# Kernel optimization log

Measured on AMD Instinct MI355X. Metric: run time of the kernel, lower is better.

Reference implementation:

```python
import jax, jax.numpy as jnp
import numpy as np

N, E, F, H, T, K = 50000, 800000, 128, 128, 10, 3


def setup_inputs() -> dict:
    key = jax.random.key(0)
    ks = jax.random.split(key, 12)
    def p(k, shape):
        return jax.random.normal(k, shape, dtype=jnp.float32) * 0.05
    inp = {
        "x": jax.random.normal(ks[0], (N, F), dtype=jnp.float32),
        "edge_index": jax.random.randint(ks[1], (2, E), 0, N, dtype=jnp.int64),
        "edge_weight": jax.random.uniform(ks[2], (E,), dtype=jnp.float32),
    }
    names = ["xz", "hz", "xr", "hr", "xh", "hh"]
    for i, nm in enumerate(names):
        cin = F if nm[0] == "x" else H
        inp["W" + nm] = p(ks[3 + i], (K, cin, H))  # ChebConv: K linear maps [in,out]
        inp["b" + nm] = jnp.zeros((H,), jnp.float32)
    inp["Wlin"] = p(ks[9], (H, T))
    inp["blin"] = jnp.zeros((T,), jnp.float32)
    return inp


def _cheb_norm(src, dst, edge_weight, n):
    # PyG ChebConv norm with normalization='sym', lambda_max=2.0:
    # L_hat = 2L/lambda_max - I = -D^{-1/2} A D^{-1/2}  (zero diagonal)
    deg = jax.ops.segment_sum(edge_weight, src, num_segments=n)
    deg_safe = jnp.where(deg > 0, deg, 1.0)
    dinv = jnp.where(deg > 0, jax.lax.rsqrt(deg_safe), 0.0)
    return -dinv[src] * edge_weight * dinv[dst]


def _cheb_conv(x, W, b, src, dst, norm, n):
    # out = sum_k T_k(L_hat) x @ W[k] + b, via Chebyshev recurrence
    def prop(t):  # L_hat @ t : gather from source nodes, scatter-add into targets
        return jax.ops.segment_sum(norm[:, None] * t[src], dst, num_segments=n)
    Tx0 = x
    out = Tx0 @ W[0]
    Tx1 = prop(Tx0)
    out = out + Tx1 @ W[1]
    for k in range(2, W.shape[0]):
        Tx2 = 2.0 * prop(Tx1) - Tx0
        out = out + Tx2 @ W[k]
        Tx0, Tx1 = Tx1, Tx2
    return out + b


def reference(x, edge_index, edge_weight, Wxz, bxz, Whz, bhz, Wxr, bxr,
              Whr, bhr, Wxh, bxh, Whh, bhh, Wlin, blin):
    n = x.shape[0]
    src, dst = edge_index[0], edge_index[1]
    norm = _cheb_norm(src, dst, edge_weight, n)
    Hs = jnp.zeros((n, Whz.shape[2]), x.dtype)  # GConvGRU inits H=None -> zeros
    Z = jax.nn.sigmoid(_cheb_conv(x, Wxz, bxz, src, dst, norm, n)
                       + _cheb_conv(Hs, Whz, bhz, src, dst, norm, n))
    R = jax.nn.sigmoid(_cheb_conv(x, Wxr, bxr, src, dst, norm, n)
                       + _cheb_conv(Hs, Whr, bhr, src, dst, norm, n))
    Ht = jnp.tanh(_cheb_conv(x, Wxh, bxh, src, dst, norm, n)
                  + _cheb_conv(Hs * R, Whh, bhh, src, dst, norm, n))
    Hn = Z * Hs + (1.0 - Z) * Ht
    return Hn @ Wlin + blin
```

## Files before the change

kernel.cpp:

```cpp
#include <hip/hip_runtime.h>
#include <hip/hip_fp16.h>

typedef __attribute__((ext_vector_type(8))) short bf16x8;
typedef __attribute__((ext_vector_type(4))) float f32x4;
typedef unsigned int u32;
typedef unsigned short u16;

#define CAP 48

static __device__ __forceinline__ u16 f2bf(float f) {
  u32 u = __float_as_uint(f);
  u32 r = (u + 0x7fffu + ((u >> 16) & 1u)) >> 16;
  return (u16)r;
}
static __device__ __forceinline__ u32 f2h15(float f) {
  __half h = __float2half(f);
  return (u32)(((__half_raw)h).x) & 0x7FFFu;
}
static __device__ __forceinline__ float h152f(u32 b) {
  __half_raw hr; hr.x = (u16)b;
  return __half2float(__half(hr));
}
static __device__ __forceinline__ void gload16(const void* g, void* l) {
  __builtin_amdgcn_global_load_lds((const __attribute__((address_space(1))) u32*)g,
                                   (__attribute__((address_space(3))) u32*)l, 16, 0, 0);
}

__global__ __launch_bounds__(256) void mega_kernel(
    const float* __restrict__ x, const int* __restrict__ ei, const float* __restrict__ w,
    const float* __restrict__ Wxz, const float* __restrict__ Wxh,
    const float* __restrict__ bxz, const float* __restrict__ bhz,
    const float* __restrict__ bxh, const float* __restrict__ bhh,
    u32* __restrict__ xw, float* __restrict__ deg, int* __restrict__ cur,
    u32* __restrict__ edges, u16* __restrict__ Bp, float* __restrict__ bzs,
    float* __restrict__ bhs, int E, int N, int nw, int eb, int pbBase, int interleave) {
  int bid = blockIdx.x, tid = threadIdx.x;
  if (bid >= pbBase) {
    int idx = (bid - pbBase) * 256 + tid;
    int j = idx & 7, h4 = (idx >> 3) & 3, n = (idx >> 5) & 15, ct = (idx >> 9) & 15, kt = idx >> 13;
    int k = kt * 32 + h4 * 8 + j;
    int c = ct * 16 + n;
    int kb = k >> 7, ci = k & 127, h = c >> 1;
    const float* W = (c & 1) ? Wxh : Wxz;
    float v = W[((size_t)kb * 128 + ci) * 128 + h];
    Bp[idx] = f2bf(v);
    if (idx < 128) { bzs[idx] = bxz[idx] + bhz[idx]; bhs[idx] = bxh[idx] + bhh[idx]; }
    return;
  }
  int role, g;
  if (interleave) { int r = bid % 6; g = bid / 6; role = (r >= 2) ? 2 : r; if (r >= 2) g = g * 4 + (r - 2); }
  else { if (bid < eb) { role = 0; g = bid; } else if (bid < 2 * eb) { role = 1; g = bid - eb; } else { role = 2; g = bid - 2 * eb; } }

  if (role == 2) {
    int i = g * 256 + tid;
    if (i < nw) {
      float2 v = *(const float2*)&x[(size_t)i * 2];
      xw[i] = (u32)f2bf(v.x) | ((u32)f2bf(v.y) << 16);
    }
  } else if (role == 0) {
    int e = g * 256 + tid;
    if (e < E) {
      int s = ei[e];
      if ((unsigned)s < (unsigned)N) atomicAdd(&deg[s], w[e]);
    }
  } else {
    int e = g * 256 + tid;
    if (e < E) {
      int s = ei[e], d = ei[E + e];
      if ((unsigned)s < (unsigned)N && (unsigned)d < (unsigned)N) {
        u32 rec = ((u32)s << 15) | f2h15(w[e]);
        int pos = atomicAdd(&cur[d], 1);
        if (pos < CAP) edges[d * CAP + pos] = rec;
      }
    }
  }
}

__global__ __launch_bounds__(256) void scale_kernel(const u32* __restrict__ xw,
                                                    const float* __restrict__ deg,
                                                    u32* __restrict__ xs, int N) {
  int node = (blockIdx.x << 2) + (threadIdx.x >> 6);
  if (node >= N) return;
  int lane = threadIdx.x & 63;
  float dd = deg[node];
  float di = dd > 0.f ? rsqrtf(dd) : 0.f;
  u32 v = xw[((unsigned)node << 6) | (unsigned)lane];
  float f0 = di * __uint_as_float(v << 16);
  float f1 = di * __uint_as_float(v & 0xffff0000u);
  xs[((unsigned)node << 6) | (unsigned)lane] = (u32)f2bf(f0) | ((u32)f2bf(f1) << 16);
}

#define ACC16(VV, NN)                                                   \
  _Pragma("unroll") for (int k_ = 0; k_ < 16; ++k_) {                   \
    a0 += NN[k_] * __uint_as_float(VV[k_] << 16);                       \
    a1 += NN[k_] * __uint_as_float(VV[k_] & 0xffff0000u);               \
  }

__global__ __launch_bounds__(256) void prop1_kernel(const u32* __restrict__ xs,
    const float* __restrict__ deg, const u32* __restrict__ edges, const int* __restrict__ cur,
    u32* __restrict__ t1w, u32* __restrict__ t1s, int N) {
  int node = (blockIdx.x << 2) + (threadIdx.x >> 6);
  if (node >= N) return;
  int lane = threadIdx.x & 63;
  int len = cur[node]; if (len > CAP) len = CAP;
  u32 my = edges[node * CAP + (lane < CAP ? lane : CAP - 1)];
  float a0 = 0.f, a1 = 0.f;
  u32 v[16]; float nv[16];
#pragma unroll
  for (int k = 0; k < 16; ++k) {
    u32 rec = (u32)__shfl((int)my, k);
    if (k < len) { v[k] = xs[((rec >> 15) << 6) | (unsigned)lane]; nv[k] = h152f(rec & 0x7FFFu); }
    else { v[k] = 0; nv[k] = 0.f; }
  }
  for (int base = 0; base < len; base += 16) {
    u32 vv[16]; float nn[16];
#pragma unroll
    for (int k = 0; k < 16; ++k) { vv[k] = v[k]; nn[k] = nv[k]; }
#pragma unroll
    for (int k = 0; k < 16; ++k) {
      int kn = base + 16 + k;
      u32 rec = (u32)__shfl((int)my, kn);
      if (kn < len) { v[k] = xs[((rec >> 15) << 6) | (unsigned)lane]; nv[k] = h152f(rec & 0x7FFFu); }
      else { v[k] = 0; nv[k] = 0.f; }
    }
    ACC16(vv, nn);
  }
  float dd = deg[node];
  float di = dd > 0.f ? rsqrtf(dd) : 0.f;
  float T0 = -di * a0, T1 = -di * a1;
  unsigned idx = ((unsigned)node << 6) | (unsigned)lane;
  t1w[idx] = (u32)f2bf(T0) | ((u32)f2bf(T1) << 16);
  t1s[idx] = (u32)f2bf(di * T0) | ((u32)f2bf(di * T1) << 16);
}

__global__ __launch_bounds__(256) void prop2_kernel(const u32* __restrict__ xw,
    const u32* __restrict__ t1s, const float* __restrict__ deg,
    const u32* __restrict__ edges, const int* __restrict__ cur,
    u32* __restrict__ t2w, int N) {
  int node = (blockIdx.x << 2) + (threadIdx.x >> 6);
  if (node >= N) return;
  int lane = threadIdx.x & 63;
  int len = cur[node]; if (len > CAP) len = CAP;
  u32 my = edges[node * CAP + (lane < CAP ? lane : CAP - 1)];
  float a0 = 0.f, a1 = 0.f;
  u32 v[16]; float nv[16];
#pragma unroll
  for (int k = 0; k < 16; ++k) {
    u32 rec = (u32)__shfl((int)my, k);
    if (k < len) { v[k] = t1s[((rec >> 15) << 6) | (unsigned)lane]; nv[k] = h152f(rec & 0x7FFFu); }
    else { v[k] = 0; nv[k] = 0.f; }
  }
  for (int base = 0; base < len; base += 16) {
    u32 vv[16]; float nn[16];
#pragma unroll
    for (int k = 0; k < 16; ++k) { vv[k] = v[k]; nn[k] = nv[k]; }
#pragma unroll
    for (int k = 0; k < 16; ++k) {
      int kn = base + 16 + k;
      u32 rec = (u32)__shfl((int)my, kn);
      if (kn < len) { v[k] = t1s[((rec >> 15) << 6) | (unsigned)lane]; nv[k] = h152f(rec & 0x7FFFu); }
      else { v[k] = 0; nv[k] = 0.f; }
    }
    ACC16(vv, nn);
  }
  float dd = deg[node];
  float di = dd > 0.f ? rsqrtf(dd) : 0.f;
  unsigned idx = ((unsigned)node << 6) | (unsigned)lane;
  u32 xv = xw[idx];
  float r0 = -2.f * di * a0 - __uint_as_float(xv << 16);
  float r1 = -2.f * di * a1 - __uint_as_float(xv & 0xffff0000u);
  t2w[idx] = (u32)f2bf(r0) | ((u32)f2bf(r1) << 16);
}

__global__ __launch_bounds__(512, 2) void gemm_kernel(
    const u16* __restrict__ xb, const u16* __restrict__ t1, const u16* __restrict__ t2,
    const u16* __restrict__ Bp, const float* __restrict__ bzs, const float* __restrict__ bhs,
    const float* __restrict__ Wlin, const float* __restrict__ blin,
    float* __restrict__ out, int N) {
  __shared__ __align__(16) char smem[49152];
  const int offB_[2] = {0, 16384};
  const int offA_[2] = {32768, 40960};

  int tid = threadIdx.x;
  int w = tid >> 6, lane = tid & 63;
  int l15 = lane & 15, lh = lane >> 4;
  int rowBase = blockIdx.x << 7;
  int wrow = (w >> 2) << 6;
  int wcol = (w & 3) << 6;

  const u16* acts[3] = {xb, t1, t2};

  f32x4 acc[4][4];
  f32x4 zero = {0.f, 0.f, 0.f, 0.f};
#pragma unroll
  for (int mi = 0; mi < 4; ++mi)
#pragma unroll
    for (int ni = 0; ni < 4; ++ni) acc[mi][ni] = zero;

  auto stageB = [&](int kt, int buf) {
    const char* g = (const char*)Bp + kt * 16384 + w * 2048 + lane * 16;
    char* l = smem + offB_[buf] + w * 2048;
    gload16(g, l);
    gload16(g + 1024, l + 1024);
  };
  auto stageA = [&](int kt, int buf) {
    int kb = kt >> 2;
    const u16* act = acts[kb];
    int rl = (w << 4) + (lane >> 2);
    int grow = rowBase + rl; if (grow >= N) grow = N - 1;
    int hsw = (lane & 3) ^ ((rl >> 1) & 3);
    const char* g = (const char*)act + (size_t)grow * 256 + ((kt & 3) << 6) + (hsw << 4);
    char* l = smem + offA_[buf] + (w << 10);
    gload16(g, l);
  };

  stageB(0, 0); stageA(0, 0);

#pragma unroll
  for (int kt = 0; kt < 12; ++kt) {
    __syncthreads();
    if (kt < 11) { stageB(kt + 1, (kt + 1) & 1); stageA(kt + 1, (kt + 1) & 1); }
    const char* Ab = smem + offA_[kt & 1];
    const char* Bb = smem + offB_[kt & 1];
    bf16x8 a[4], b[4];
#pragma unroll
    for (int mi = 0; mi < 4; ++mi) {
      int row = wrow + (mi << 4) + l15;
      int off = (row << 6) + ((lh ^ ((row >> 1) & 3)) << 4);
      a[mi] = *(const bf16x8*)(Ab + off);
    }
#pragma unroll
    for (int ni = 0; ni < 4; ++ni) {
      int ct = ((w & 3) << 2) + ni;
      int off = (((ct << 4) + l15) << 6) + (lh << 4);
      b[ni] = *(const bf16x8*)(Bb + off);
    }
#pragma unroll
    for (int mi = 0; mi < 4; ++mi)
#pragma unroll
      for (int ni = 0; ni < 4; ++ni)
        acc[mi][ni] = __builtin_amdgcn_mfma_f32_16x16x32_bf16(a[mi], b[ni], acc[mi][ni], 0, 0, 0);
  }

  __syncthreads();

  u16* HnS = (u16*)smem;
  float* WlS = (float*)(smem + 34816);
  float* blS = (float*)(smem + 34816 + 5120);
  for (int i = tid; i < 1280; i += 512) WlS[i] = Wlin[i];
  if (tid < 10) blS[tid] = blin[tid];

  int odd = lane & 1;
#pragma unroll
  for (int ni = 0; ni < 4; ++ni) {
    int h = (wcol + (ni << 4) + l15) >> 1;
    float badd = odd ? bhs[h] : bzs[h];
#pragma unroll
    for (int mi = 0; mi < 4; ++mi)
#pragma unroll
      for (int reg = 0; reg < 4; ++reg) {
        float pre = acc[mi][ni][reg] + badd;
        float s2 = odd ? 2.f * pre : pre;
        float e = __expf(s2);
        float A = odd ? 1.f : 0.f;
        float B = odd ? 2.f : -1.f;
        float r = A - B / (1.f + e);
        float o = __shfl_xor(r, 1);
        if (!odd) {
          int row = wrow + (mi << 4) + (lh << 2) + reg;
          HnS[row * 136 + h] = f2bf(r * o);
        }
      }
  }
  __syncthreads();

  for (int idx = tid; idx < 1280; idx += 512) {
    int row = idx / 10, t = idx - row * 10;
    int grow = rowBase + row;
    if (grow < N) {
      float s = blS[t];
      const u16* hr = HnS + row * 136;
#pragma unroll 4
      for (int hc = 0; hc < 16; ++hc) {
        uint4 q = *(const uint4*)(hr + (hc << 3));
        const float* wp = WlS + (hc << 3) * 10 + t;
        s += __uint_as_float(q.x << 16) * wp[0];
        s += __uint_as_float(q.x & 0xffff0000u) * wp[10];
        s += __uint_as_float(q.y << 16) * wp[20];
        s += __uint_as_float(q.y & 0xffff0000u) * wp[30];
        s += __uint_as_float(q.z << 16) * wp[40];
        s += __uint_as_float(q.z & 0xffff0000u) * wp[50];
        s += __uint_as_float(q.w << 16) * wp[60];
        s += __uint_as_float(q.w & 0xffff0000u) * wp[70];
      }
      out[(size_t)grow * 10 + t] = s;
    }
  }
}

extern "C" void kernel_launch(void* const* d_in, const int* in_sizes, int n_in,
                              void* d_out, int out_size, void* d_ws, size_t ws_size,
                              hipStream_t stream) {
  const float* x    = (const float*)d_in[0];
  const int*   ei   = (const int*)d_in[1];
  const float* w    = (const float*)d_in[2];
  const float* Wxz  = (const float*)d_in[3];
  const float* bxz  = (const float*)d_in[4];
  const float* bhz  = (const float*)d_in[6];
  const float* Wxh  = (const float*)d_in[11];
  const float* bxh  = (const float*)d_in[12];
  const float* bhh  = (const float*)d_in[14];
  const float* Wlin = (const float*)d_in[15];
  const float* blin = (const float*)d_in[16];
  float* out = (float*)d_out;

  int N = in_sizes[0] / 128;
  int E = in_sizes[2];

  char* p = (char*)d_ws;
  auto alloc = [&](size_t bytes) {
    char* r = p;
    p += (bytes + 255) & ~(size_t)255;
    return r;
  };
  float* deg   = (float*)alloc((size_t)N * 4);
  int*   cur   = (int*)alloc((size_t)N * 4);
  u32*   edges = (u32*)alloc((size_t)N * CAP * 4);
  u32*   xbw   = (u32*)alloc((size_t)N * 256);
  u32*   xs    = (u32*)alloc((size_t)N * 256);
  u32*   t1w   = (u32*)alloc((size_t)N * 256);
  u32*   t1s   = (u32*)alloc((size_t)N * 256);
  u32*   t2w   = (u32*)alloc((size_t)N * 256);
  u16*   Bp    = (u16*)alloc(196608);
  float* bzs   = (float*)alloc(512);
  float* bhs   = (float*)alloc(512);

  hipMemsetAsync(deg, 0, (size_t)N * 4, stream);
  hipMemsetAsync(cur, 0, (size_t)N * 4, stream);

  int nw = N * 64;
  int eb = (E + 255) / 256;
  int cb = (nw + 255) / 256;
  int interleave = (cb == 4 * eb) ? 1 : 0;
  int workB = interleave ? 6 * eb : (2 * eb + cb);
  int pbBase = workB;
  int grid = workB + 384;

  hipLaunchKernelGGL(mega_kernel, dim3(grid), dim3(256), 0, stream,
                     x, ei, w, Wxz, Wxh, bxz, bhz, bxh, bhh,
                     xbw, deg, cur, edges, Bp, bzs, bhs, E, N, nw, eb, pbBase, interleave);
  int nb = (N + 3) / 4;
  hipLaunchKernelGGL(scale_kernel, dim3(nb), dim3(256), 0, stream, xbw, deg, xs, N);
  hipLaunchKernelGGL(prop1_kernel, dim3(nb), dim3(256), 0, stream, xs, deg, edges, cur, t1w, t1s, N);
  hipLaunchKernelGGL(prop2_kernel, dim3(nb), dim3(256), 0, stream, xbw, t1s, deg, edges, cur, t2w, N);
  int gb = (N + 127) / 128;
  hipLaunchKernelGGL(gemm_kernel, dim3(gb), dim3(512), 0, stream,
                     (const u16*)xbw, (const u16*)t1w, (const u16*)t2w, Bp, bzs, bhs,
                     Wlin, blin, out, N);
}
```

Baseline: 295.5 us.

## Fold source-degree scaling into per-edge weights, drop scale kernel and t1s buffer

Each edge weight now absorbs the source node's inverse sqrt degree, computed once per lane before the gather loop. The propagation kernels can then read the unscaled bf16 features directly. This removes the separate scale pass, the pre-scaled xs copy, and the second t1s output write, which cuts one launch and several full N×128 bf16 read/write passes. It also merges the two memsets into one. In exchange, each edge does a random deg lookup and an rsqrt, and the rounding order changes slightly.

```diff
diff --git a/kernel.cpp b/kernel.cpp
--- a/kernel.cpp
+++ b/kernel.cpp
@@ -76,40 +76,30 @@
   }
 }
 
-__global__ __launch_bounds__(256) void scale_kernel(const u32* __restrict__ xw,
-                                                    const float* __restrict__ deg,
-                                                    u32* __restrict__ xs, int N) {
-  int node = (blockIdx.x << 2) + (threadIdx.x >> 6);
-  if (node >= N) return;
-  int lane = threadIdx.x & 63;
-  float dd = deg[node];
-  float di = dd > 0.f ? rsqrtf(dd) : 0.f;
-  u32 v = xw[((unsigned)node << 6) | (unsigned)lane];
-  float f0 = di * __uint_as_float(v << 16);
-  float f1 = di * __uint_as_float(v & 0xffff0000u);
-  xs[((unsigned)node << 6) | (unsigned)lane] = (u32)f2bf(f0) | ((u32)f2bf(f1) << 16);
-}
-
 #define ACC16(VV, NN)                                                   \
   _Pragma("unroll") for (int k_ = 0; k_ < 16; ++k_) {                   \
     a0 += NN[k_] * __uint_as_float(VV[k_] << 16);                       \
     a1 += NN[k_] * __uint_as_float(VV[k_] & 0xffff0000u);               \
   }
 
-__global__ __launch_bounds__(256) void prop1_kernel(const u32* __restrict__ xs,
+__global__ __launch_bounds__(256) void prop1_kernel(const u32* __restrict__ xw,
     const float* __restrict__ deg, const u32* __restrict__ edges, const int* __restrict__ cur,
-    u32* __restrict__ t1w, u32* __restrict__ t1s, int N) {
+    u32* __restrict__ t1w, int N) {
   int node = (blockIdx.x << 2) + (threadIdx.x >> 6);
   if (node >= N) return;
   int lane = threadIdx.x & 63;
   int len = cur[node]; if (len > CAP) len = CAP;
-  u32 my = edges[node * CAP + (lane < CAP ? lane : CAP - 1)];
+  u32 rec = edges[node * CAP + (lane < CAP ? lane : CAP - 1)];
+  u32 sbase = (rec >> 15) << 6;
+  float dgs = (lane < len) ? deg[rec >> 15] : 1.f;
+  float nvl = (lane < len && dgs > 0.f) ? h152f(rec & 0x7FFFu) * rsqrtf(dgs) : 0.f;
   float a0 = 0.f, a1 = 0.f;
   u32 v[16]; float nv[16];
 #pragma unroll
   for (int k = 0; k < 16; ++k) {
-    u32 rec = (u32)__shfl((int)my, k);
-    if (k < len) { v[k] = xs[((rec >> 15) << 6) | (unsigned)lane]; nv[k] = h152f(rec & 0x7FFFu); }
+    u32 sb = (u32)__shfl((int)sbase, k);
+    float n = __shfl(nvl, k);
+    if (k < len) { v[k] = xw[sb | (unsigned)lane]; nv[k] = n; }
     else { v[k] = 0; nv[k] = 0.f; }
   }
   for (int base = 0; base < len; base += 16) {
@@ -119,35 +109,38 @@
 #pragma unroll
     for (int k = 0; k < 16; ++k) {
       int kn = base + 16 + k;
-      u32 rec = (u32)__shfl((int)my, kn);
-      if (kn < len) { v[k] = xs[((rec >> 15) << 6) | (unsigned)lane]; nv[k] = h152f(rec & 0x7FFFu); }
+      u32 sb = (u32)__shfl((int)sbase, kn);
+      float n = __shfl(nvl, kn);
+      if (kn < len) { v[k] = xw[sb | (unsigned)lane]; nv[k] = n; }
       else { v[k] = 0; nv[k] = 0.f; }
     }
     ACC16(vv, nn);
   }
   float dd = deg[node];
-  float di = dd > 0.f ? rsqrtf(dd) : 0.f;
-  float T0 = -di * a0, T1 = -di * a1;
+  float di = dd > 0.f ? -rsqrtf(dd) : 0.f;
   unsigned idx = ((unsigned)node << 6) | (unsigned)lane;
-  t1w[idx] = (u32)f2bf(T0) | ((u32)f2bf(T1) << 16);
-  t1s[idx] = (u32)f2bf(di * T0) | ((u32)f2bf(di * T1) << 16);
+  t1w[idx] = (u32)f2bf(di * a0) | ((u32)f2bf(di * a1) << 16);
 }
 
 __global__ __launch_bounds__(256) void prop2_kernel(const u32* __restrict__ xw,
-    const u32* __restrict__ t1s, const float* __restrict__ deg,
+    const u32* __restrict__ t1w, const float* __restrict__ deg,
     const u32* __restrict__ edges, const int* __restrict__ cur,
     u32* __restrict__ t2w, int N) {
   int node = (blockIdx.x << 2) + (threadIdx.x >> 6);
   if (node >= N) return;
   int lane = threadIdx.x & 63;
   int len = cur[node]; if (len > CAP) len = CAP;
-  u32 my = edges[node * CAP + (lane < CAP ? lane : CAP - 1)];
+  u32 rec = edges[node * CAP + (lane < CAP ? lane : CAP - 1)];
+  u32 sbase = (rec >> 15) << 6;
+  float dgs = (lane < len) ? deg[rec >> 15] : 1.f;
+  float nvl = (lane < len && dgs > 0.f) ? h152f(rec & 0x7FFFu) * rsqrtf(dgs) : 0.f;
   float a0 = 0.f, a1 = 0.f;
   u32 v[16]; float nv[16];
 #pragma unroll
   for (int k = 0; k < 16; ++k) {
-    u32 rec = (u32)__shfl((int)my, k);
-    if (k < len) { v[k] = t1s[((rec >> 15) << 6) | (unsigned)lane]; nv[k] = h152f(rec & 0x7FFFu); }
+    u32 sb = (u32)__shfl((int)sbase, k);
+    float n = __shfl(nvl, k);
+    if (k < len) { v[k] = t1w[sb | (unsigned)lane]; nv[k] = n; }
     else { v[k] = 0; nv[k] = 0.f; }
   }
   for (int base = 0; base < len; base += 16) {
@@ -157,8 +150,9 @@
 #pragma unroll
     for (int k = 0; k < 16; ++k) {
       int kn = base + 16 + k;
-      u32 rec = (u32)__shfl((int)my, kn);
-      if (kn < len) { v[k] = t1s[((rec >> 15) << 6) | (unsigned)lane]; nv[k] = h152f(rec & 0x7FFFu); }
+      u32 sb = (u32)__shfl((int)sbase, kn);
+      float n = __shfl(nvl, kn);
+      if (kn < len) { v[k] = t1w[sb | (unsigned)lane]; nv[k] = n; }
       else { v[k] = 0; nv[k] = 0.f; }
     }
     ACC16(vv, nn);
@@ -323,20 +317,17 @@
     p += (bytes + 255) & ~(size_t)255;
     return r;
   };
-  float* deg   = (float*)alloc((size_t)N * 4);
-  int*   cur   = (int*)alloc((size_t)N * 4);
+  float* deg   = (float*)alloc((size_t)N * 8);
+  int*   cur   = (int*)(deg + N);
   u32*   edges = (u32*)alloc((size_t)N * CAP * 4);
   u32*   xbw   = (u32*)alloc((size_t)N * 256);
-  u32*   xs    = (u32*)alloc((size_t)N * 256);
   u32*   t1w   = (u32*)alloc((size_t)N * 256);
-  u32*   t1s   = (u32*)alloc((size_t)N * 256);
   u32*   t2w   = (u32*)alloc((size_t)N * 256);
   u16*   Bp    = (u16*)alloc(196608);
   float* bzs   = (float*)alloc(512);
   float* bhs   = (float*)alloc(512);
 
-  hipMemsetAsync(deg, 0, (size_t)N * 4, stream);
-  hipMemsetAsync(cur, 0, (size_t)N * 4, stream);
+  hipMemsetAsync(deg, 0, (size_t)N * 8, stream);
 
   int nw = N * 64;
   int eb = (E + 255) / 256;
@@ -350,9 +341,8 @@
                      x, ei, w, Wxz, Wxh, bxz, bhz, bxh, bhh,
                      xbw, deg, cur, edges, Bp, bzs, bhs, E, N, nw, eb, pbBase, interleave);
   int nb = (N + 3) / 4;
-  hipLaunchKernelGGL(scale_kernel, dim3(nb), dim3(256), 0, stream, xbw, deg, xs, N);
-  hipLaunchKernelGGL(prop1_kernel, dim3(nb), dim3(256), 0, stream, xs, deg, edges, cur, t1w, t1s, N);
-  hipLaunchKernelGGL(prop2_kernel, dim3(nb), dim3(256), 0, stream, xbw, t1s, deg, edges, cur, t2w, N);
+  hipLaunchKernelGGL(prop1_kernel, dim3(nb), dim3(256), 0, stream, xbw, deg, edges, cur, t1w, N);
+  hipLaunchKernelGGL(prop2_kernel, dim3(nb), dim3(256), 0, stream, xbw, t1w, deg, edges, cur, t2w, N);
   int gb = (N + 127) / 128;
   hipLaunchKernelGGL(gemm_kernel, dim3(gb), dim3(512), 0, stream,
                      (const u16*)xbw, (const u16*)t1w, (const u16*)t2w, Bp, bzs, bhs,
```

Result: slower. 302.6 us (+2.4%).
